# Kernel tuning notes

Measured on AMD Instinct MI355X. Metric: run time of the kernel, lower is better.

## Reference

```python
import jax, jax.numpy as jnp
import numpy as np

B, T, CTX, D, L, H, FF, NMODES = 1024, 512, 23, 320, 5, 8, 1280, 48
DH = D // H
EPS = 1e-5


def layernorm(x, w, b):
    m = jnp.mean(x, axis=-1, keepdims=True)
    v = jnp.mean(jnp.square(x - m), axis=-1, keepdims=True)
    return (x - m) * jax.lax.rsqrt(v + EPS) * w + b


def cheb_sum(x, c):
    """sum_n c[:, n] * T_n(x) via the Chebyshev recurrence, fused with the
    reduction (Clenshaw-style accumulation, no (B,T,N+1) intermediate).
    x: (B,T) in [-1,1], c: (B, N+1)."""
    t_prev = jnp.ones_like(x)           # T_0
    t_cur = x                           # T_1
    acc = c[:, 0:1] * t_prev + c[:, 1:2] * t_cur

    def step(carry, cn):
        tp, tc, a = carry
        tn = 2.0 * x * tc - tp          # T_{n+1}
        return (tc, tn, a + cn[:, None] * tn), None

    (_, _, acc), _ = jax.lax.scan(step, (t_prev, t_cur, acc),
                                  jnp.swapaxes(c[:, 2:], 0, 1))
    return acc


def _forward(k_norm, ctx, W_e, b_e, cls, ln1_w, ln1_b, W_in, b_in, W_out, b_out,
             ln2_w, ln2_b, W1, b1, W2, b2, hln_w, hln_b, Wh1, bh1, Wh2, bh2):
    Bc = ctx.shape[0]
    # elem_proj: Linear(1, D) applied per scalar token -> (B, CTX, D)
    tok = ctx[..., None] * W_e + b_e
    x = jnp.concatenate([jnp.broadcast_to(cls, (Bc, 1, D)), tok], axis=1)  # (B, 24, D)

    def layer(x, p):
        l1w, l1b, win, bin_, wout, bout, l2w, l2b, w1, b1_, w2, b2_ = p
        # --- pre-norm self attention ---
        h = layernorm(x, l1w, l1b)
        qkv = h @ win.T + bin_                      # (B, S, 3D)
        q, k, v = jnp.split(qkv, 3, axis=-1)
        S = x.shape[1]
        q = q.reshape(Bc, S, H, DH)
        k = k.reshape(Bc, S, H, DH)
        v = v.reshape(Bc, S, H, DH)
        scores = jnp.einsum('bqhd,bkhd->bhqk', q, k) / np.sqrt(DH).astype(np.float32)
        a = jax.nn.softmax(scores, axis=-1)
        o = jnp.einsum('bhqk,bkhd->bqhd', a, v).reshape(Bc, S, D)
        x = x + o @ wout.T + bout
        # --- pre-norm FFN ---
        h2 = layernorm(x, l2w, l2b)
        x = x + jax.nn.gelu(h2 @ w1.T + b1_, approximate=False) @ w2.T + b2_
        return x, None

    x, _ = jax.lax.scan(layer, x, (ln1_w, ln1_b, W_in, b_in, W_out, b_out,
                                   ln2_w, ln2_b, W1, b1, W2, b2))
    h = layernorm(x[:, 0], hln_w, hln_b)            # CLS pooling + head LN
    c = jax.nn.gelu(h @ Wh1.T + bh1, approximate=False) @ Wh2.T + bh2  # (B, N+1)
    z = cheb_sum(k_norm, c)
    return jax.nn.sigmoid(z)


def setup_inputs() -> dict:
    key = jax.random.key(0)
    ks = jax.random.split(key, 24)
    rn = lambda k, sh, s=0.02: jax.random.normal(k, sh, jnp.float32) * s
    return {
        'k_norm': jax.random.uniform(ks[0], (B, T), jnp.float32, -1.0, 1.0),
        'ctx': jax.random.normal(ks[1], (B, CTX), jnp.float32),
        'W_e': rn(ks[2], (D,), 0.5),
        'b_e': jnp.zeros((D,), jnp.float32),
        'cls': rn(ks[3], (1, 1, D)),
        'ln1_w': jnp.ones((L, D), jnp.float32),
        'ln1_b': jnp.zeros((L, D), jnp.float32),
        'W_in': rn(ks[4], (L, 3 * D, D)),
        'b_in': jnp.zeros((L, 3 * D), jnp.float32),
        'W_out': rn(ks[5], (L, D, D)),
        'b_out': jnp.zeros((L, D), jnp.float32),
        'ln2_w': jnp.ones((L, D), jnp.float32),
        'ln2_b': jnp.zeros((L, D), jnp.float32),
        'W1': rn(ks[6], (L, FF, D)),
        'b1': jnp.zeros((L, FF), jnp.float32),
        'W2': rn(ks[7], (L, D, FF)),
        'b2': jnp.zeros((L, D), jnp.float32),
        'hln_w': jnp.ones((D,), jnp.float32),
        'hln_b': jnp.zeros((D,), jnp.float32),
        'Wh1': rn(ks[8], (D, D)),
        'bh1': jnp.zeros((D,), jnp.float32),
        'Wh2': rn(ks[9], (NMODES + 1, D)),
        'bh2': jnp.zeros((NMODES + 1,), jnp.float32),
    }


def reference(k_norm, ctx, W_e, b_e, cls, ln1_w, ln1_b, W_in, b_in, W_out, b_out,
              ln2_w, ln2_b, W1, b1, W2, b2, hln_w, hln_b, Wh1, bh1, Wh2, bh2):
    return _forward(k_norm, ctx, W_e, b_e, cls, ln1_w, ln1_b, W_in, b_in, W_out,
                    b_out, ln2_w, ln2_b, W1, b1, W2, b2, hln_w, hln_b, Wh1, bh1,
                    Wh2, bh2)
```

## Files before the change

kernel.cpp:

```cpp
#include <hip/hip_runtime.h>
#include <hip/hip_bf16.h>
#include <math.h>

#define B_SZ 1024
#define T_SZ 512
#define CTX_N 23
#define D 320
#define L_LAYERS 5
#define H 8
#define FF 1280
#define NM1 49
#define S 24
#define DH 40
#define M_ROWS (B_SZ * S)

typedef unsigned short ushort_t;
typedef __attribute__((ext_vector_type(8))) short bfrag8;
typedef __attribute__((ext_vector_type(4))) float facc4;

__device__ __forceinline__ float wave_sum(float v) {
#pragma unroll
  for (int off = 32; off > 0; off >>= 1) v += __shfl_xor(v, off, 64);
  return v;
}

__device__ __forceinline__ float gelu_fast(float x) {
  float t = __builtin_amdgcn_exp2f(x * (2.30211416f + 0.10294404f * x * x));
  return x - x * __builtin_amdgcn_rcpf(t + 1.0f);
}

__device__ __forceinline__ ushort_t f2b(float x) {
  __hip_bfloat16 h = __float2bfloat16(x);
  return *reinterpret_cast<ushort_t*>(&h);
}

__device__ __forceinline__ float b2f(ushort_t u) {
  __hip_bfloat16 h = *reinterpret_cast<__hip_bfloat16*>(&u);
  return __bfloat162float(h);
}

#define GLOAD_LDS16(g, l)                                     \
  __builtin_amdgcn_global_load_lds(                           \
      (const __attribute__((address_space(1))) void*)(g),     \
      (__attribute__((address_space(3))) void*)(l), 16, 0, 0)

__global__ __launch_bounds__(256) void conv_all(
    const float* __restrict__ w_in, const float* __restrict__ w_out,
    const float* __restrict__ w1, const float* __restrict__ w2,
    const float* __restrict__ wh1, ushort_t* __restrict__ dst) {
  int i = blockIdx.x * 256 + threadIdx.x;
  const float* src;
  int off;
  if (i < 384000)       { src = w_in;  off = i; }
  else if (i < 512000)  { src = w_out; off = i - 384000; }
  else if (i < 1024000) { src = w1;    off = i - 512000; }
  else if (i < 1536000) { src = w2;    off = i - 1024000; }
  else                  { src = wh1;   off = i - 1536000; }
  float4 v = ((const float4*)src)[off];
  ushort4 o;
  o.x = f2b(v.x); o.y = f2b(v.y); o.z = f2b(v.z); o.w = f2b(v.w);
  ((ushort4*)dst)[i] = o;
}

__global__ __launch_bounds__(256) void embed_kernel(
    const float* __restrict__ ctx, const float* __restrict__ W_e,
    const float* __restrict__ b_e, const float* __restrict__ cls,
    float* __restrict__ x) {
  int idx = blockIdx.x * 256 + threadIdx.x;
  int d = idx % D;
  int s = (idx / D) % S;
  int b = idx / (D * S);
  float v;
  if (s == 0)
    v = cls[d];
  else
    v = ctx[b * CTX_N + (s - 1)] * W_e[d] + b_e[d];
  x[idx] = v;
}

__global__ __launch_bounds__(256) void ln_kernel(
    const float* __restrict__ X, const float* __restrict__ w,
    const float* __restrict__ b, ushort_t* __restrict__ Y,
    int inStride, int outStride) {
  int wv = threadIdx.x >> 6;
  int lane = threadIdx.x & 63;
  int row = blockIdx.x * 4 + wv;
  const float* xr = X + (size_t)row * inStride;
  float v[5];
#pragma unroll
  for (int i = 0; i < 5; i++) v[i] = xr[lane + 64 * i];
  float s = v[0] + v[1] + v[2] + v[3] + v[4];
  s = wave_sum(s);
  float m = s * (1.0f / (float)D);
  float sq = 0.f;
#pragma unroll
  for (int i = 0; i < 5; i++) { float d0 = v[i] - m; sq += d0 * d0; }
  sq = wave_sum(sq);
  float inv = 1.0f / sqrtf(sq * (1.0f / (float)D) + 1e-5f);
  ushort_t* yr = Y + (size_t)row * outStride;
#pragma unroll
  for (int i = 0; i < 5; i++) {
    int d = lane + 64 * i;
    yr[d] = f2b((v[i] - m) * inv * w[d] + b[d]);
  }
}

template <int EPI, int BM_, int NT>
__global__ __launch_bounds__(256, 3) void gemm_mfma(
    const ushort_t* __restrict__ A, const ushort_t* __restrict__ W,
    const float* __restrict__ bias, const float* __restrict__ R,
    float* __restrict__ C, ushort_t* __restrict__ Cb, int M, int N, int K) {
  constexpr int BK = 64;
  constexpr int BN = 32 * NT;
  constexpr int MT = BM_ / 32;
  constexpr int AR = BM_ / 32;
  constexpr int WR = BN / 32;
  __shared__ __align__(16) ushort_t As[BM_ * BK];
  __shared__ __align__(16) ushort_t Ws[BN * BK];

  int tid = threadIdx.x;
  int lane = tid & 63;
  int wv = tid >> 6;
  int wvM = wv & 1, wvN = wv >> 1;
  int laneM = lane & 15;
  int kgrp = lane >> 4;
  int sA = laneM & 7;
  int m0 = blockIdx.x * BM_;
  int n0 = blockIdx.y * BN;

  facc4 acc[MT][NT];
#pragma unroll
  for (int mt = 0; mt < MT; mt++)
#pragma unroll
    for (int nt = 0; nt < NT; nt++) acc[mt][nt] = (facc4){0.f, 0.f, 0.f, 0.f};

  int srow = tid >> 3;
  int jg = (tid & 7) ^ (srow & 7);
  const ushort_t* Ag = A + (size_t)(m0 + srow) * K + jg * 8;
  const ushort_t* Wg = W + (size_t)(n0 + srow) * K + jg * 8;

  for (int k0 = 0; k0 < K; k0 += BK) {
#pragma unroll
    for (int r = 0; r < AR; r++)
      GLOAD_LDS16(Ag + (size_t)r * 32 * K + k0, As + r * 2048 + tid * 8);
#pragma unroll
    for (int r = 0; r < WR; r++)
      GLOAD_LDS16(Wg + (size_t)r * 32 * K + k0, Ws + r * 2048 + tid * 8);
    __syncthreads();
#pragma unroll
    for (int kc = 0; kc < 2; kc++) {
      int jcol = ((kc * 4 + kgrp) ^ sA) * 8;
      bfrag8 af[MT];
#pragma unroll
      for (int mt = 0; mt < MT; mt++) {
        int row = wvM * (BM_ / 2) + mt * 16 + laneM;
        af[mt] = *(const bfrag8*)&As[row * 64 + jcol];
      }
      bfrag8 bf[NT];
#pragma unroll
      for (int nt = 0; nt < NT; nt++) {
        int nrow = wvN * (BN / 2) + nt * 16 + laneM;
        bf[nt] = *(const bfrag8*)&Ws[nrow * 64 + jcol];
      }
#pragma unroll
      for (int mt = 0; mt < MT; mt++)
#pragma unroll
        for (int nt = 0; nt < NT; nt++)
          acc[mt][nt] = __builtin_amdgcn_mfma_f32_16x16x32_bf16(
              bf[nt], af[mt], acc[mt][nt], 0, 0, 0);
    }
    __syncthreads();
  }

#pragma unroll
  for (int mt = 0; mt < MT; mt++) {
    int m = m0 + wvM * (BM_ / 2) + mt * 16 + laneM;
#pragma unroll
    for (int nt = 0; nt < NT; nt++) {
      int n = n0 + wvN * (BN / 2) + nt * 16 + kgrp * 4;
      float4 bv = *(const float4*)(bias + n);
      facc4 a = acc[mt][nt];
      float v0 = a[0] + bv.x, v1 = a[1] + bv.y, v2 = a[2] + bv.z,
            v3 = a[3] + bv.w;
      size_t off = (size_t)m * N + n;
      if constexpr (EPI == 1) {
        ushort4 o;
        o.x = f2b(gelu_fast(v0)); o.y = f2b(gelu_fast(v1));
        o.z = f2b(gelu_fast(v2)); o.w = f2b(gelu_fast(v3));
        *(ushort4*)(Cb + off) = o;
      } else if constexpr (EPI == 2) {
        float4 r = *(const float4*)(R + off);
        float4 o = {v0 + r.x, v1 + r.y, v2 + r.z, v3 + r.w};
        *(float4*)(C + off) = o;
      } else if constexpr (EPI == 3) {
        float4 o = {gelu_fast(v0), gelu_fast(v1), gelu_fast(v2),
                    gelu_fast(v3)};
        *(float4*)(C + off) = o;
      } else {
        ushort4 o;
        o.x = f2b(v0); o.y = f2b(v1); o.z = f2b(v2); o.w = f2b(v3);
        *(ushort4*)(Cb + off) = o;
      }
    }
  }
}

__global__ __launch_bounds__(256) void attn_kernel(
    const ushort_t* __restrict__ qkv, ushort_t* __restrict__ o) {
  int b = blockIdx.x >> 3;
  int h = blockIdx.x & 7;
  __shared__ __align__(16) float q[S][44];
  __shared__ __align__(16) float v[S][44];
  __shared__ __align__(16) float kT[DH][28];
  __shared__ __align__(16) float sc[S][28];
  int tid = threadIdx.x;
  const ushort_t* base = qkv + (size_t)b * S * (3 * D) + h * DH;

  for (int idx = tid; idx < 720; idx += 256) {
    int t = idx / 240;
    int r = idx % 240;
    int s = r / 10, dg = r % 10;
    ushort4 u = *(const ushort4*)(base + (size_t)s * (3 * D) + t * D + dg * 4);
    float4 f = {b2f(u.x), b2f(u.y), b2f(u.z), b2f(u.w)};
    if (t == 0) {
      *(float4*)&q[s][dg * 4] = f;
    } else if (t == 2) {
      *(float4*)&v[s][dg * 4] = f;
    } else {
      kT[dg * 4 + 0][s] = f.x;
      kT[dg * 4 + 1][s] = f.y;
      kT[dg * 4 + 2][s] = f.z;
      kT[dg * 4 + 3][s] = f.w;
    }
  }
  __syncthreads();

  if (tid < 144) {
    int i = tid / 6, jg = tid % 6;
    facc4 acc = {0.f, 0.f, 0.f, 0.f};
#pragma unroll
    for (int d = 0; d < DH; d++) {
      float qv = q[i][d];
      float4 kv = *(const float4*)&kT[d][jg * 4];
      acc[0] += qv * kv.x; acc[1] += qv * kv.y;
      acc[2] += qv * kv.z; acc[3] += qv * kv.w;
    }
    const float sca = 0.15811388300841897f;
    float4 ov = {acc[0] * sca, acc[1] * sca, acc[2] * sca, acc[3] * sca};
    *(float4*)&sc[i][jg * 4] = ov;
  }
  __syncthreads();

  if (tid < S) {
    float mx = -1e30f;
#pragma unroll
    for (int j = 0; j < S; j++) mx = fmaxf(mx, sc[tid][j]);
    float sum = 0.f;
#pragma unroll
    for (int j = 0; j < S; j++) {
      float e = __expf(sc[tid][j] - mx);
      sc[tid][j] = e;
      sum += e;
    }
    float rr = 1.0f / sum;
#pragma unroll
    for (int j = 0; j < S; j++) sc[tid][j] *= rr;
  }
  __syncthreads();

  if (tid < 240) {
    int i = tid / 10, dg = tid % 10;
    facc4 acc = {0.f, 0.f, 0.f, 0.f};
#pragma unroll
    for (int j = 0; j < S; j++) {
      float p = sc[i][j];
      float4 vv = *(const float4*)&v[j][dg * 4];
      acc[0] += p * vv.x; acc[1] += p * vv.y;
      acc[2] += p * vv.z; acc[3] += p * vv.w;
    }
    ushort4 ov;
    ov.x = f2b(acc[0]); ov.y = f2b(acc[1]);
    ov.z = f2b(acc[2]); ov.w = f2b(acc[3]);
    *(ushort4*)(o + (size_t)b * S * D + (size_t)i * D + h * DH + dg * 4) = ov;
  }
}

__global__ __launch_bounds__(256) void head_cheb(
    const float* __restrict__ g, const float* __restrict__ Wh2,
    const float* __restrict__ bh2, const float* __restrict__ k_norm,
    float* __restrict__ out) {
  int b = blockIdx.x;
  __shared__ float gs[D];
  __shared__ float cs[NM1];
  int tid = threadIdx.x;
  for (int i = tid; i < D; i += 256) gs[i] = g[(size_t)b * D + i];
  __syncthreads();
  if (tid < NM1) {
    const float* wr = Wh2 + (size_t)tid * D;
    float s = bh2[tid];
    for (int d = 0; d < D; d++) s += gs[d] * wr[d];
    cs[tid] = s;
  }
  __syncthreads();
  for (int t = tid; t < T_SZ; t += 256) {
    float xv = k_norm[(size_t)b * T_SZ + t];
    float tp = 1.f, tc = xv;
    float acc = cs[0] + cs[1] * xv;
#pragma unroll
    for (int n = 2; n < NM1; n++) {
      float tn = 2.f * xv * tc - tp;
      acc += cs[n] * tn;
      tp = tc;
      tc = tn;
    }
    out[(size_t)b * T_SZ + t] = 1.f / (1.f + expf(-acc));
  }
}

extern "C" void kernel_launch(void* const* d_in, const int* in_sizes, int n_in,
                              void* d_out, int out_size, void* d_ws,
                              size_t ws_size, hipStream_t stream) {
  const float* k_norm = (const float*)d_in[0];
  const float* ctx    = (const float*)d_in[1];
  const float* W_e    = (const float*)d_in[2];
  const float* b_e    = (const float*)d_in[3];
  const float* cls    = (const float*)d_in[4];
  const float* ln1_w  = (const float*)d_in[5];
  const float* ln1_b  = (const float*)d_in[6];
  const float* W_in   = (const float*)d_in[7];
  const float* b_in   = (const float*)d_in[8];
  const float* W_out  = (const float*)d_in[9];
  const float* b_out  = (const float*)d_in[10];
  const float* ln2_w  = (const float*)d_in[11];
  const float* ln2_b  = (const float*)d_in[12];
  const float* W1     = (const float*)d_in[13];
  const float* b1     = (const float*)d_in[14];
  const float* W2     = (const float*)d_in[15];
  const float* b2     = (const float*)d_in[16];
  const float* hln_w  = (const float*)d_in[17];
  const float* hln_b  = (const float*)d_in[18];
  const float* Wh1    = (const float*)d_in[19];
  const float* bh1    = (const float*)d_in[20];
  const float* Wh2    = (const float*)d_in[21];
  const float* bh2    = (const float*)d_in[22];
  float* out = (float*)d_out;

  float* x = (float*)d_ws;
  ushort_t* hbuf = (ushort_t*)(x + (size_t)M_ROWS * D);
  ushort_t* big = hbuf + (size_t)M_ROWS * D;
  ushort_t* wb_in = big + (size_t)M_ROWS * FF;
  ushort_t* wb_out = wb_in + (size_t)L_LAYERS * 3 * D * D;
  ushort_t* wb1 = wb_out + (size_t)L_LAYERS * D * D;
  ushort_t* wb2 = wb1 + (size_t)L_LAYERS * FF * D;
  ushort_t* wbh1 = wb2 + (size_t)L_LAYERS * D * FF;
  ushort_t* hcls = wbh1 + (size_t)D * D;
  float* ghead = (float*)(hcls + (size_t)B_SZ * D);

  conv_all<<<6100, 256, 0, stream>>>(W_in, W_out, W1, W2, Wh1, wb_in);

  embed_kernel<<<(M_ROWS * D) / 256, 256, 0, stream>>>(ctx, W_e, b_e, cls, x);

  for (int l = 0; l < L_LAYERS; l++) {
    ln_kernel<<<M_ROWS / 4, 256, 0, stream>>>(x, ln1_w + l * D, ln1_b + l * D,
                                              hbuf, D, D);
    gemm_mfma<4, 64, 5><<<dim3(M_ROWS / 64, (3 * D) / 160), 256, 0, stream>>>(
        hbuf, wb_in + (size_t)l * 3 * D * D, b_in + (size_t)l * 3 * D, nullptr,
        nullptr, big, M_ROWS, 3 * D, D);
    attn_kernel<<<B_SZ * H, 256, 0, stream>>>(big, hbuf);
    gemm_mfma<2, 64, 5><<<dim3(M_ROWS / 64, D / 160), 256, 0, stream>>>(
        hbuf, wb_out + (size_t)l * D * D, b_out + (size_t)l * D, x, x, nullptr,
        M_ROWS, D, D);
    ln_kernel<<<M_ROWS / 4, 256, 0, stream>>>(x, ln2_w + l * D, ln2_b + l * D,
                                              hbuf, D, D);
    gemm_mfma<1, 64, 5><<<dim3(M_ROWS / 64, FF / 160), 256, 0, stream>>>(
        hbuf, wb1 + (size_t)l * FF * D, b1 + (size_t)l * FF, nullptr, nullptr,
        big, M_ROWS, FF, D);
    gemm_mfma<2, 64, 5><<<dim3(M_ROWS / 64, D / 160), 256, 0, stream>>>(
        big, wb2 + (size_t)l * D * FF, b2 + (size_t)l * D, x, x, nullptr,
        M_ROWS, D, FF);
  }

  ln_kernel<<<B_SZ / 4, 256, 0, stream>>>(x, hln_w, hln_b, hcls, S * D, D);
  gemm_mfma<3, 64, 5><<<dim3(B_SZ / 64, D / 160), 256, 0, stream>>>(
      hcls, wbh1, bh1, nullptr, ghead, nullptr, B_SZ, D, D);
  head_cheb<<<B_SZ, 256, 0, stream>>>(ghead, Wh2, bh2, k_norm, out);
}
```

Before: 1.002 ms.

## Fuse LayerNorm into GEMM prologue using row stats from residual epilogues

Removes the standalone LayerNorm kernels inside each layer. The residual GEMM epilogues (and the embedding kernel) now accumulate per-row sum and sum-of-squares with atomics into a stats buffer. The QKV and FFN1 GEMMs read fp32 x directly, apply the normalization, convert to bf16 and store into LDS. This avoids a full bf16 activation write and read per LayerNorm, but the A tile now comes from fp32 global loads instead of async LDS loads. It also uses a one-pass E[x^2]-mean^2 variance, which is less numerically stable, plus atomics and an extra memset.

```diff
diff --git a/kernel.cpp b/kernel.cpp
--- a/kernel.cpp
+++ b/kernel.cpp
@@ -16,6 +16,7 @@
 
 typedef unsigned short ushort_t;
 typedef __attribute__((ext_vector_type(8))) short bfrag8;
+typedef __attribute__((ext_vector_type(8))) unsigned short us8v;
 typedef __attribute__((ext_vector_type(4))) float facc4;
 
 __device__ __forceinline__ float wave_sum(float v) {
@@ -62,20 +63,31 @@
   ((ushort4*)dst)[i] = o;
 }
 
-__global__ __launch_bounds__(256) void embed_kernel(
+__global__ __launch_bounds__(256) void embed_stats(
     const float* __restrict__ ctx, const float* __restrict__ W_e,
     const float* __restrict__ b_e, const float* __restrict__ cls,
-    float* __restrict__ x) {
-  int idx = blockIdx.x * 256 + threadIdx.x;
-  int d = idx % D;
-  int s = (idx / D) % S;
-  int b = idx / (D * S);
-  float v;
-  if (s == 0)
-    v = cls[d];
-  else
-    v = ctx[b * CTX_N + (s - 1)] * W_e[d] + b_e[d];
-  x[idx] = v;
+    float* __restrict__ x, float* __restrict__ stats) {
+  int wvi = threadIdx.x >> 6;
+  int lane = threadIdx.x & 63;
+  int row = blockIdx.x * 4 + wvi;
+  int b = row / S, s = row % S;
+  float c = (s == 0) ? 0.f : ctx[b * CTX_N + (s - 1)];
+  float* xr = x + (size_t)row * D;
+  float vs = 0.f, vq = 0.f;
+#pragma unroll
+  for (int i = 0; i < 5; i++) {
+    int d = lane + 64 * i;
+    float v = (s == 0) ? cls[d] : c * W_e[d] + b_e[d];
+    xr[d] = v;
+    vs += v;
+    vq += v * v;
+  }
+  vs = wave_sum(vs);
+  vq = wave_sum(vq);
+  if (lane == 0) {
+    stats[2 * row] = vs;
+    stats[2 * row + 1] = vq;
+  }
 }
 
 __global__ __launch_bounds__(256) void ln_kernel(
@@ -109,7 +121,8 @@
 __global__ __launch_bounds__(256, 3) void gemm_mfma(
     const ushort_t* __restrict__ A, const ushort_t* __restrict__ W,
     const float* __restrict__ bias, const float* __restrict__ R,
-    float* __restrict__ C, ushort_t* __restrict__ Cb, int M, int N, int K) {
+    float* __restrict__ C, ushort_t* __restrict__ Cb,
+    float* __restrict__ stats, int M, int N, int K) {
   constexpr int BK = 64;
   constexpr int BN = 32 * NT;
   constexpr int MT = BM_ / 32;
@@ -175,6 +188,7 @@
 #pragma unroll
   for (int mt = 0; mt < MT; mt++) {
     int m = m0 + wvM * (BM_ / 2) + mt * 16 + laneM;
+    float rs = 0.f, rq = 0.f;
 #pragma unroll
     for (int nt = 0; nt < NT; nt++) {
       int n = n0 + wvN * (BN / 2) + nt * 16 + kgrp * 4;
@@ -183,24 +197,147 @@
       float v0 = a[0] + bv.x, v1 = a[1] + bv.y, v2 = a[2] + bv.z,
             v3 = a[3] + bv.w;
       size_t off = (size_t)m * N + n;
-      if constexpr (EPI == 1) {
-        ushort4 o;
-        o.x = f2b(gelu_fast(v0)); o.y = f2b(gelu_fast(v1));
-        o.z = f2b(gelu_fast(v2)); o.w = f2b(gelu_fast(v3));
-        *(ushort4*)(Cb + off) = o;
-      } else if constexpr (EPI == 2) {
+      if constexpr (EPI == 2 || EPI == 6) {
         float4 r = *(const float4*)(R + off);
         float4 o = {v0 + r.x, v1 + r.y, v2 + r.z, v3 + r.w};
         *(float4*)(C + off) = o;
+        if constexpr (EPI == 6) {
+          rs += o.x + o.y + o.z + o.w;
+          rq += o.x * o.x + o.y * o.y + o.z * o.z + o.w * o.w;
+        }
       } else if constexpr (EPI == 3) {
         float4 o = {gelu_fast(v0), gelu_fast(v1), gelu_fast(v2),
                     gelu_fast(v3)};
         *(float4*)(C + off) = o;
+      }
+    }
+    if constexpr (EPI == 6) {
+      rs += __shfl_xor(rs, 16, 64);
+      rs += __shfl_xor(rs, 32, 64);
+      rq += __shfl_xor(rq, 16, 64);
+      rq += __shfl_xor(rq, 32, 64);
+      if (kgrp == 0) {
+        atomicAdd(stats + 2 * m, rs);
+        atomicAdd(stats + 2 * m + 1, rq);
+      }
+    }
+  }
+}
+
+template <int EPI, int NT>
+__global__ __launch_bounds__(256, 3) void gemm_ln(
+    const float* __restrict__ Xf, const ushort_t* __restrict__ W,
+    const float* __restrict__ lnw, const float* __restrict__ lnb,
+    const float* __restrict__ stats, const float* __restrict__ bias,
+    ushort_t* __restrict__ Cb, int M, int N, int K) {
+  constexpr int BM_ = 64, BK = 64;
+  constexpr int BN = 32 * NT;
+  constexpr int MT = 2;
+  constexpr int WR = BN / 32;
+  __shared__ __align__(16) ushort_t As[BM_ * BK];
+  __shared__ __align__(16) ushort_t Ws[BN * BK];
+
+  int tid = threadIdx.x;
+  int lane = tid & 63;
+  int wv = tid >> 6;
+  int wvM = wv & 1, wvN = wv >> 1;
+  int laneM = lane & 15;
+  int kgrp = lane >> 4;
+  int sA = laneM & 7;
+  int m0 = blockIdx.x * BM_;
+  int n0 = blockIdx.y * BN;
+
+  facc4 acc[MT][NT];
+#pragma unroll
+  for (int mt = 0; mt < MT; mt++)
+#pragma unroll
+    for (int nt = 0; nt < NT; nt++) acc[mt][nt] = (facc4){0.f, 0.f, 0.f, 0.f};
+
+  int srow = tid >> 3;
+  int jg = (tid & 7) ^ (srow & 7);
+  const float* Xg = Xf + (size_t)(m0 + srow) * K + jg * 8;
+  const ushort_t* Wg = W + (size_t)(n0 + srow) * K + jg * 8;
+
+  float alpha[2], beta[2];
+#pragma unroll
+  for (int r = 0; r < 2; r++) {
+    int row = m0 + srow + r * 32;
+    float sm = stats[2 * row] * (1.0f / (float)D);
+    float sq = stats[2 * row + 1] * (1.0f / (float)D);
+    float rstd = rsqrtf(sq - sm * sm + 1e-5f);
+    alpha[r] = rstd;
+    beta[r] = -sm * rstd;
+  }
+
+  for (int k0 = 0; k0 < K; k0 += BK) {
+#pragma unroll
+    for (int r = 0; r < WR; r++)
+      GLOAD_LDS16(Wg + (size_t)r * 32 * K + k0, Ws + r * 2048 + tid * 8);
+    const float4* wp = (const float4*)(lnw + k0 + jg * 8);
+    const float4* bp = (const float4*)(lnb + k0 + jg * 8);
+    float4 w0 = wp[0], w1 = wp[1];
+    float4 c0 = bp[0], c1 = bp[1];
+#pragma unroll
+    for (int r = 0; r < 2; r++) {
+      const float4* xp = (const float4*)(Xg + (size_t)r * 32 * K + k0);
+      float4 x0 = xp[0], x1 = xp[1];
+      float al = alpha[r], be = beta[r];
+      us8v u;
+      u[0] = f2b(fmaf(fmaf(x0.x, al, be), w0.x, c0.x));
+      u[1] = f2b(fmaf(fmaf(x0.y, al, be), w0.y, c0.y));
+      u[2] = f2b(fmaf(fmaf(x0.z, al, be), w0.z, c0.z));
+      u[3] = f2b(fmaf(fmaf(x0.w, al, be), w0.w, c0.w));
+      u[4] = f2b(fmaf(fmaf(x1.x, al, be), w1.x, c1.x));
+      u[5] = f2b(fmaf(fmaf(x1.y, al, be), w1.y, c1.y));
+      u[6] = f2b(fmaf(fmaf(x1.z, al, be), w1.z, c1.z));
+      u[7] = f2b(fmaf(fmaf(x1.w, al, be), w1.w, c1.w));
+      *(us8v*)&As[r * 2048 + tid * 8] = u;
+    }
+    __syncthreads();
+#pragma unroll
+    for (int kc = 0; kc < 2; kc++) {
+      int jcol = ((kc * 4 + kgrp) ^ sA) * 8;
+      bfrag8 af[MT];
+#pragma unroll
+      for (int mt = 0; mt < MT; mt++) {
+        int row = wvM * 32 + mt * 16 + laneM;
+        af[mt] = *(const bfrag8*)&As[row * 64 + jcol];
+      }
+      bfrag8 bf[NT];
+#pragma unroll
+      for (int nt = 0; nt < NT; nt++) {
+        int nrow = wvN * (BN / 2) + nt * 16 + laneM;
+        bf[nt] = *(const bfrag8*)&Ws[nrow * 64 + jcol];
+      }
+#pragma unroll
+      for (int mt = 0; mt < MT; mt++)
+#pragma unroll
+        for (int nt = 0; nt < NT; nt++)
+          acc[mt][nt] = __builtin_amdgcn_mfma_f32_16x16x32_bf16(
+              bf[nt], af[mt], acc[mt][nt], 0, 0, 0);
+    }
+    __syncthreads();
+  }
+
+#pragma unroll
+  for (int mt = 0; mt < MT; mt++) {
+    int m = m0 + wvM * 32 + mt * 16 + laneM;
+#pragma unroll
+    for (int nt = 0; nt < NT; nt++) {
+      int n = n0 + wvN * (BN / 2) + nt * 16 + kgrp * 4;
+      float4 bv = *(const float4*)(bias + n);
+      facc4 a = acc[mt][nt];
+      float v0 = a[0] + bv.x, v1 = a[1] + bv.y, v2 = a[2] + bv.z,
+            v3 = a[3] + bv.w;
+      size_t off = (size_t)m * N + n;
+      ushort4 o;
+      if constexpr (EPI == 1) {
+        o.x = f2b(gelu_fast(v0)); o.y = f2b(gelu_fast(v1));
+        o.z = f2b(gelu_fast(v2)); o.w = f2b(gelu_fast(v3));
       } else {
-        ushort4 o;
         o.x = f2b(v0); o.y = f2b(v1); o.z = f2b(v2); o.w = f2b(v3);
-        *(ushort4*)(Cb + off) = o;
-      }
+      }
+      *(ushort4*)(Cb + off) = o;
     }
   }
 }
@@ -355,33 +492,37 @@
   ushort_t* wbh1 = wb2 + (size_t)L_LAYERS * D * FF;
   ushort_t* hcls = wbh1 + (size_t)D * D;
   float* ghead = (float*)(hcls + (size_t)B_SZ * D);
+  float* sQ = ghead + (size_t)B_SZ * D;
+  float* sB = sQ + (size_t)6 * M_ROWS * 2;
+
+  hipMemsetAsync(sQ + (size_t)M_ROWS * 2, 0,
+                 (size_t)10 * M_ROWS * 2 * sizeof(float), stream);
 
   conv_all<<<6100, 256, 0, stream>>>(W_in, W_out, W1, W2, Wh1, wb_in);
 
-  embed_kernel<<<(M_ROWS * D) / 256, 256, 0, stream>>>(ctx, W_e, b_e, cls, x);
+  embed_stats<<<M_ROWS / 4, 256, 0, stream>>>(ctx, W_e, b_e, cls, x, sQ);
 
   for (int l = 0; l < L_LAYERS; l++) {
-    ln_kernel<<<M_ROWS / 4, 256, 0, stream>>>(x, ln1_w + l * D, ln1_b + l * D,
-                                              hbuf, D, D);
-    gemm_mfma<4, 64, 5><<<dim3(M_ROWS / 64, (3 * D) / 160), 256, 0, stream>>>(
-        hbuf, wb_in + (size_t)l * 3 * D * D, b_in + (size_t)l * 3 * D, nullptr,
-        nullptr, big, M_ROWS, 3 * D, D);
+    float* stQ = sQ + (size_t)l * M_ROWS * 2;
+    float* stB = sB + (size_t)l * M_ROWS * 2;
+    float* stN = sQ + (size_t)(l + 1) * M_ROWS * 2;
+    gemm_ln<4, 5><<<dim3(M_ROWS / 64, (3 * D) / 160), 256, 0, stream>>>(
+        x, wb_in + (size_t)l * 3 * D * D, ln1_w + l * D, ln1_b + l * D, stQ,
+        b_in + (size_t)l * 3 * D, big, M_ROWS, 3 * D, D);
     attn_kernel<<<B_SZ * H, 256, 0, stream>>>(big, hbuf);
-    gemm_mfma<2, 64, 5><<<dim3(M_ROWS / 64, D / 160), 256, 0, stream>>>(
+    gemm_mfma<6, 64, 5><<<dim3(M_ROWS / 64, D / 160), 256, 0, stream>>>(
         hbuf, wb_out + (size_t)l * D * D, b_out + (size_t)l * D, x, x, nullptr,
-        M_ROWS, D, D);
-    ln_kernel<<<M_ROWS / 4, 256, 0, stream>>>(x, ln2_w + l * D, ln2_b + l * D,
-                                              hbuf, D, D);
-    gemm_mfma<1, 64, 5><<<dim3(M_ROWS / 64, FF / 160), 256, 0, stream>>>(
-        hbuf, wb1 + (size_t)l * FF * D, b1 + (size_t)l * FF, nullptr, nullptr,
-        big, M_ROWS, FF, D);
-    gemm_mfma<2, 64, 5><<<dim3(M_ROWS / 64, D / 160), 256, 0, stream>>>(
-        big, wb2 + (size_t)l * D * FF, b2 + (size_t)l * D, x, x, nullptr,
+        stB, M_ROWS, D, D);
+    gemm_ln<1, 5><<<dim3(M_ROWS / 64, FF / 160), 256, 0, stream>>>(
+        x, wb1 + (size_t)l * FF * D, ln2_w + l * D, ln2_b + l * D, stB,
+        b1 + (size_t)l * FF, big, M_ROWS, FF, D);
+    gemm_mfma<6, 64, 5><<<dim3(M_ROWS / 64, D / 160), 256, 0, stream>>>(
+        big, wb2 + (size_t)l * D * FF, b2 + (size_t)l * D, x, x, nullptr, stN,
         M_ROWS, D, FF);
   }
 
   ln_kernel<<<B_SZ / 4, 256, 0, stream>>>(x, hln_w, hln_b, hcls, S * D, D);
   gemm_mfma<3, 64, 5><<<dim3(B_SZ / 64, D / 160), 256, 0, stream>>>(
-      hcls, wbh1, bh1, nullptr, ghead, nullptr, B_SZ, D, D);
+      hcls, wbh1, bh1, nullptr, ghead, nullptr, nullptr, B_SZ, D, D);
   head_cheb<<<B_SZ, 256, 0, stream>>>(ghead, Wh2, bh2, k_norm, out);
 }
```

Measured after the change: 1.045 ms. +4.3%, slower.
